# Performance work log

Hardware: AMD Instinct MI355X
Metric: run time of the kernel (lower is better)

Reference implementation:

```python
import jax, jax.numpy as jnp
import numpy as np

COST_CLASS = 1.0
COST_REG = 1.0
NUM_TGT = 5  # targets per batch element, implied by `sizes = [5] * ...`

# All 5^5 = 3125 ways for each of the 5 targets to pick one of its 5 cheapest queries.
_CHOICES = np.stack(np.meshgrid(*([np.arange(NUM_TGT)] * NUM_TGT), indexing='ij'), -1).reshape(-1, NUM_TGT)


def _solve_lap5(cost):
    """Exact rectangular linear_sum_assignment for cost [num_queries, 5].

    Exchange argument: some optimal matching assigns every target (column) to one of
    its 5 cheapest queries (at most 4 of them can be taken by the other targets).
    So enumerate 5^5 candidate tuples, mask duplicates, take the argmin.
    Returns (row_ind, col_ind) sorted by row like scipy.linear_sum_assignment.
    """
    neg_vals, idx = jax.lax.top_k(-cost.T, NUM_TGT)          # [5 targets, 5 candidates]
    vals = -neg_vals
    choices = jnp.asarray(_CHOICES)                          # [3125, 5]
    t = jnp.arange(NUM_TGT)
    cand_q = idx[t[None, :], choices]                        # [3125, 5] query index per target
    cand_c = vals[t[None, :], choices]                       # [3125, 5] matching cost per target
    sq = jnp.sort(cand_q, axis=-1)
    valid = jnp.all(sq[:, 1:] != sq[:, :-1], axis=-1)        # all chosen queries distinct
    total = jnp.where(valid, cand_c.sum(-1), jnp.inf)
    best = jnp.argmin(total)
    rows = cand_q[best]                                      # [5] query index per target 0..4
    order = jnp.argsort(rows)
    return rows[order].astype(jnp.int32), order.astype(jnp.int32)


def setup_inputs() -> dict:
    key = jax.random.key(0)
    k1, k2, k3, k4 = jax.random.split(key, 4)
    bs, nq, T = 32, 2048, 32 * NUM_TGT
    return {
        'pred_logits': jax.random.normal(k1, (bs, nq, 1), dtype=jnp.float32),
        'pred_regs': jax.random.normal(k2, (bs, nq, 3), dtype=jnp.float32),
        'labels': jax.random.randint(k3, (T,), 0, 2, dtype=jnp.int32),
        'tgt_regression': jax.random.normal(k4, (T, 3), dtype=jnp.float32),
    }


def reference(pred_logits, pred_regs, labels, tgt_regression):
    bs, nq = pred_logits.shape[:2]
    # out_prob = softmax(pred_logits) is computed in the original but never used
    # (and tgt labels are unused): classification cost reduces to the constant cost_class.
    out_bbox = pred_regs.reshape(bs * nq, 3)
    # L1 cdist against ALL targets, as in the original: [bs*nq, T]
    cost_reg = jnp.sum(jnp.abs(out_bbox[:, None, :] - tgt_regression[None, :, :]), axis=-1)
    C = COST_REG * cost_reg + COST_CLASS
    # split the target axis into per-batch blocks of 5 and keep the diagonal block
    C = C.reshape(bs, nq, bs, NUM_TGT)
    b = jnp.arange(bs)
    Cb = C[b, :, b, :]                                       # [bs, nq, 5]
    rows, cols = jax.vmap(_solve_lap5)(Cb)                   # each [bs, 5]
    return rows, cols
```

## Files before the change

### kernel.cpp

```cpp
#include <hip/hip_runtime.h>

#define NUM_TGT 5

__device__ __forceinline__ bool lex_less(float c1, int q1, float c2, int q2) {
    return (c1 < c2) || (c1 == c2 && q1 < q2);
}

__device__ __forceinline__ void insert5(float c[5], int q[5], float cv, int qv) {
    if (lex_less(cv, qv, c[4], q[4])) {
        c[4] = cv; q[4] = qv;
#pragma unroll
        for (int i = 3; i >= 0; --i) {
            if (lex_less(c[i + 1], q[i + 1], c[i], q[i])) {
                float tc = c[i]; c[i] = c[i + 1]; c[i + 1] = tc;
                int   tq = q[i]; q[i] = q[i + 1]; q[i + 1] = tq;
            }
        }
    }
}

__global__ __launch_bounds__(320)
void hungarian_match_kernel(const float* __restrict__ pred_regs,
                            const float* __restrict__ tgt_reg,
                            int* __restrict__ out,
                            int nq, int bs) {
    const int b    = blockIdx.x;
    const int tid  = threadIdx.x;
    const int wave = tid >> 6;
    const int lane = tid & 63;

    __shared__ float top_c[NUM_TGT][NUM_TGT];
    __shared__ int   top_q[NUM_TGT][NUM_TGT];
    __shared__ float red_t[NUM_TGT];
    __shared__ int   red_k[NUM_TGT];

    {
        const int t = wave;
        const float t0 = tgt_reg[(b * NUM_TGT + t) * 3 + 0];
        const float t1 = tgt_reg[(b * NUM_TGT + t) * 3 + 1];
        const float t2 = tgt_reg[(b * NUM_TGT + t) * 3 + 2];

        float c[5] = {INFINITY, INFINITY, INFINITY, INFINITY, INFINITY};
        int   q[5] = {0x7fffffff, 0x7fffffff, 0x7fffffff, 0x7fffffff, 0x7fffffff};

        const float* base = pred_regs + (size_t)b * nq * 3;
        for (int j = 0; j * 64 + lane < nq; ++j) {
            const int qi = j * 64 + lane;
            float cost = fabsf(base[qi * 3 + 0] - t0);
            cost = cost + fabsf(base[qi * 3 + 1] - t1);
            cost = cost + fabsf(base[qi * 3 + 2] - t2);
            cost = cost + 1.0f;
            insert5(c, q, cost, qi);
        }

#pragma unroll
        for (int m = 1; m < 64; m <<= 1) {
#pragma unroll
            for (int i = 0; i < 5; ++i) {
                float oc = __shfl_xor(c[i], m, 64);
                int   oq = __shfl_xor(q[i], m, 64);
                insert5(c, q, oc, oq);
            }
        }

        if (lane == 0) {
#pragma unroll
            for (int i = 0; i < 5; ++i) { top_c[t][i] = c[i]; top_q[t][i] = q[i]; }
        }
    }
    __syncthreads();

    float bt = INFINITY;
    int   bk = 0x7fffffff;
    for (int k = tid; k < 3125; k += 320) {
        int r  = k;
        const int d0 = r / 625; r -= d0 * 625;
        const int d1 = r / 125; r -= d1 * 125;
        const int d2 = r / 25;  r -= d2 * 25;
        const int d3 = r / 5;
        const int d4 = r - d3 * 5;

        const int q0 = top_q[0][d0], q1 = top_q[1][d1], q2 = top_q[2][d2],
                  q3 = top_q[3][d3], q4 = top_q[4][d4];
        const bool valid =
            q0 != q1 && q0 != q2 && q0 != q3 && q0 != q4 &&
            q1 != q2 && q1 != q3 && q1 != q4 &&
            q2 != q3 && q2 != q4 &&
            q3 != q4;

        float tot = top_c[0][d0];
        tot = tot + top_c[1][d1];
        tot = tot + top_c[2][d2];
        tot = tot + top_c[3][d3];
        tot = tot + top_c[4][d4];
        if (!valid) tot = INFINITY;

        if (tot < bt || (tot == bt && k < bk)) { bt = tot; bk = k; }
    }

#pragma unroll
    for (int off = 32; off; off >>= 1) {
        float ot = __shfl_down(bt, off, 64);
        int   ok = __shfl_down(bk, off, 64);
        if (ot < bt || (ot == bt && ok < bk)) { bt = ot; bk = ok; }
    }
    if (lane == 0) { red_t[wave] = bt; red_k[wave] = bk; }
    __syncthreads();

    if (tid == 0) {
        float fbt = red_t[0]; int fbk = red_k[0];
#pragma unroll
        for (int w = 1; w < NUM_TGT; ++w) {
            if (red_t[w] < fbt || (red_t[w] == fbt && red_k[w] < fbk)) {
                fbt = red_t[w]; fbk = red_k[w];
            }
        }
        int r = fbk;
        int d[5];
        d[0] = r / 625; r -= d[0] * 625;
        d[1] = r / 125; r -= d[1] * 125;
        d[2] = r / 25;  r -= d[2] * 25;
        d[3] = r / 5;
        d[4] = r - d[3] * 5;

        int rows[5];
#pragma unroll
        for (int t = 0; t < 5; ++t) rows[t] = top_q[t][d[t]];

#pragma unroll
        for (int i = 0; i < 5; ++i) {
            int rank = 0;
#pragma unroll
            for (int j = 0; j < 5; ++j) rank += (rows[j] < rows[i]);
            out[b * 5 + rank]          = rows[i];
            out[bs * 5 + b * 5 + rank] = i;
        }
    }
}

extern "C" void kernel_launch(void* const* d_in, const int* in_sizes, int n_in,
                              void* d_out, int out_size, void* d_ws, size_t ws_size,
                              hipStream_t stream) {
    const float* pred_regs = (const float*)d_in[1];
    const float* tgt_reg   = (const float*)d_in[3];
    int* out = (int*)d_out;

    const int T  = in_sizes[2];
    const int bs = T / NUM_TGT;
    const int nq = in_sizes[0] / bs;

    hungarian_match_kernel<<<bs, 320, 0, stream>>>(pred_regs, tgt_reg, out, nq, bs);
}
```

Baseline: 83.46 us.

## Split matcher into parallel per-target top-k kernel and enumeration kernel

```diff
diff --git a/kernel.cpp b/kernel.cpp
--- a/kernel.cpp
+++ b/kernel.cpp
@@ -19,11 +19,76 @@
     }
 }
 
-__global__ __launch_bounds__(320)
-void hungarian_match_kernel(const float* __restrict__ pred_regs,
-                            const float* __restrict__ tgt_reg,
-                            int* __restrict__ out,
-                            int nq, int bs) {
+__global__ __launch_bounds__(256)
+void topk_kernel(const float* __restrict__ pred_regs,
+                 const float* __restrict__ tgt_reg,
+                 float* __restrict__ ws_c,
+                 int* __restrict__ ws_q,
+                 int nq) {
+    const int bt   = blockIdx.x;
+    const int b    = bt / NUM_TGT;
+    const int tid  = threadIdx.x;
+    const int wave = tid >> 6;
+    const int lane = tid & 63;
+
+    __shared__ float wc[4][NUM_TGT];
+    __shared__ int   wq[4][NUM_TGT];
+
+    const float t0 = tgt_reg[bt * 3 + 0];
+    const float t1 = tgt_reg[bt * 3 + 1];
+    const float t2 = tgt_reg[bt * 3 + 2];
+
+    float c[5] = {INFINITY, INFINITY, INFINITY, INFINITY, INFINITY};
+    int   q[5] = {0x7fffffff, 0x7fffffff, 0x7fffffff, 0x7fffffff, 0x7fffffff};
+
+    const float* base = pred_regs + (size_t)b * nq * 3;
+#pragma unroll
+    for (int j = 0; j < 8; ++j) {
+        const int qi = j * 256 + tid;
+        if (qi < nq) {
+            float cost = fabsf(base[qi * 3 + 0] - t0);
+            cost = cost + fabsf(base[qi * 3 + 1] - t1);
+            cost = cost + fabsf(base[qi * 3 + 2] - t2);
+            cost = cost + 1.0f;
+            insert5(c, q, cost, qi);
+        }
+    }
+
+#pragma unroll
+    for (int m = 1; m < 64; m <<= 1) {
+#pragma unroll
+        for (int i = 0; i < 5; ++i) {
+            float oc = __shfl_xor(c[i], m, 64);
+            int   oq = __shfl_xor(q[i], m, 64);
+            insert5(c, q, oc, oq);
+        }
+    }
+
+    if (lane == 0) {
+#pragma unroll
+        for (int i = 0; i < 5; ++i) { wc[wave][i] = c[i]; wq[wave][i] = q[i]; }
+    }
+    __syncthreads();
+
+    if (tid == 0) {
+#pragma unroll
+        for (int w = 1; w < 4; ++w)
+#pragma unroll
+            for (int i = 0; i < 5; ++i)
+                insert5(c, q, wc[w][i], wq[w][i]);
+#pragma unroll
+        for (int i = 0; i < 5; ++i) {
+            ws_c[bt * NUM_TGT + i] = c[i];
+            ws_q[bt * NUM_TGT + i] = q[i];
+        }
+    }
+}
+
+__global__ __launch_bounds__(256)
+void enumerate_kernel(const float* __restrict__ ws_c,
+                      const int* __restrict__ ws_q,
+                      int* __restrict__ out,
+                      int bs) {
     const int b    = blockIdx.x;
     const int tid  = threadIdx.x;
     const int wave = tid >> 6;
@@ -31,48 +96,18 @@
 
     __shared__ float top_c[NUM_TGT][NUM_TGT];
     __shared__ int   top_q[NUM_TGT][NUM_TGT];
-    __shared__ float red_t[NUM_TGT];
-    __shared__ int   red_k[NUM_TGT];
+    __shared__ float red_t[4];
+    __shared__ int   red_k[4];
 
-    {
-        const int t = wave;
-        const float t0 = tgt_reg[(b * NUM_TGT + t) * 3 + 0];
-        const float t1 = tgt_reg[(b * NUM_TGT + t) * 3 + 1];
-        const float t2 = tgt_reg[(b * NUM_TGT + t) * 3 + 2];
-
-        float c[5] = {INFINITY, INFINITY, INFINITY, INFINITY, INFINITY};
-        int   q[5] = {0x7fffffff, 0x7fffffff, 0x7fffffff, 0x7fffffff, 0x7fffffff};
-
-        const float* base = pred_regs + (size_t)b * nq * 3;
-        for (int j = 0; j * 64 + lane < nq; ++j) {
-            const int qi = j * 64 + lane;
-            float cost = fabsf(base[qi * 3 + 0] - t0);
-            cost = cost + fabsf(base[qi * 3 + 1] - t1);
-            cost = cost + fabsf(base[qi * 3 + 2] - t2);
-            cost = cost + 1.0f;
-            insert5(c, q, cost, qi);
-        }
-
-#pragma unroll
-        for (int m = 1; m < 64; m <<= 1) {
-#pragma unroll
-            for (int i = 0; i < 5; ++i) {
-                float oc = __shfl_xor(c[i], m, 64);
-                int   oq = __shfl_xor(q[i], m, 64);
-                insert5(c, q, oc, oq);
-            }
-        }
-
-        if (lane == 0) {
-#pragma unroll
-            for (int i = 0; i < 5; ++i) { top_c[t][i] = c[i]; top_q[t][i] = q[i]; }
-        }
+    if (tid < 25) {
+        top_c[tid / 5][tid % 5] = ws_c[b * 25 + tid];
+        top_q[tid / 5][tid % 5] = ws_q[b * 25 + tid];
     }
     __syncthreads();
 
     float bt = INFINITY;
     int   bk = 0x7fffffff;
-    for (int k = tid; k < 3125; k += 320) {
+    for (int k = tid; k < 3125; k += 256) {
         int r  = k;
         const int d0 = r / 625; r -= d0 * 625;
         const int d1 = r / 125; r -= d1 * 125;
@@ -110,7 +145,7 @@
     if (tid == 0) {
         float fbt = red_t[0]; int fbk = red_k[0];
 #pragma unroll
-        for (int w = 1; w < NUM_TGT; ++w) {
+        for (int w = 1; w < 4; ++w) {
             if (red_t[w] < fbt || (red_t[w] == fbt && red_k[w] < fbk)) {
                 fbt = red_t[w]; fbk = red_k[w];
             }
@@ -149,5 +184,9 @@
     const int bs = T / NUM_TGT;
     const int nq = in_sizes[0] / bs;
 
-    hungarian_match_kernel<<<bs, 320, 0, stream>>>(pred_regs, tgt_reg, out, nq, bs);
+    float* ws_c = (float*)d_ws;
+    int*   ws_q = (int*)(ws_c + (size_t)bs * NUM_TGT * NUM_TGT);
+
+    topk_kernel<<<bs * NUM_TGT, 256, 0, stream>>>(pred_regs, tgt_reg, ws_c, ws_q, nq);
+    enumerate_kernel<<<bs, 256, 0, stream>>>(ws_c, ws_q, out, bs);
 }
```

After: 75.26 us. -9.8%, faster.
